# Kernel tuning notes

Measured on AMD Instinct MI355X. Metric: run time of the kernel, lower is better.

The kernel has to match this reference:

```python
import jax, jax.numpy as jnp
import numpy as np

B, N, D, H, NCTX = 4, 2048, 1024, 16, 512
HD = D // H  # head dim = 64


def setup_inputs() -> dict:
    key = jax.random.key(0)
    ks = jax.random.split(key, 6)
    return {
        "x": jax.random.normal(ks[0], (B, N, D), dtype=jnp.float32),
        "ctx_ppr": jax.random.uniform(ks[1], (B, NCTX), dtype=jnp.float32),
        "ctx_trust": jax.random.normal(ks[2], (B, NCTX), dtype=jnp.float32),
        "W_in": jax.random.normal(ks[3], (D, 3 * D), dtype=jnp.float32) * 0.02,
        "b_in": jnp.zeros((3 * D,), dtype=jnp.float32),
        "W_out": jax.random.normal(ks[4], (D, D), dtype=jnp.float32) * 0.02,
        "b_out": jnp.zeros((D,), dtype=jnp.float32),
        "log_ppr_alpha": jnp.full((1,), 0.1, dtype=jnp.float32),
        "trust_scale": jnp.full((1,), 0.1, dtype=jnp.float32),
        "n_ctx": NCTX,
    }


def reference(x, ctx_ppr, ctx_trust, W_in, b_in, W_out, b_out, log_ppr_alpha, trust_scale, n_ctx):
    b, n, dmodel = x.shape
    # QKV projection
    qkv = x @ W_in + b_in                                   # [B,N,3D]
    q, k, v = jnp.split(qkv, 3, axis=-1)
    q = q.reshape(b, n, H, HD).transpose(0, 2, 1, 3)        # [B,H,N,d]
    k = k.reshape(b, n, H, HD).transpose(0, 2, 1, 3)
    v = v.reshape(b, n, H, HD).transpose(0, 2, 1, 3)
    if n_ctx > 0:
        # multiplicative trust gate on context-token values
        gate = jax.nn.sigmoid(trust_scale * ctx_trust)      # [B,n_ctx]
        gate_full = jnp.concatenate(
            [gate, jnp.ones((b, n - n_ctx), dtype=x.dtype)], axis=1)  # [B,N]
        v = v * gate_full[:, None, :, None]
        # additive graph (log-PPR) column bias on attention logits
        col_bias = -log_ppr_alpha * jnp.log(jnp.maximum(ctx_ppr, 1e-8))  # [B,n_ctx]
        bias = jnp.concatenate(
            [col_bias, jnp.zeros((b, n - n_ctx), dtype=x.dtype)], axis=1)  # [B,N]
    else:
        bias = jnp.zeros((b, n), dtype=x.dtype)
    scale = 1.0 / np.sqrt(HD).astype(np.float32)
    scores = jnp.einsum("bhqd,bhkd->bhqk", q, k) * scale + bias[:, None, None, :]
    attn = jax.nn.softmax(scores, axis=-1)                  # [B,H,N,N]
    out = jnp.einsum("bhqk,bhkd->bhqd", attn, v)            # [B,H,N,d]
    out = out.transpose(0, 2, 1, 3).reshape(b, n, dmodel)
    return out @ W_out + b_out
```

## Files before the change

### kernel.cpp

```cpp
#include <hip/hip_runtime.h>
#include <hip/hip_bf16.h>
#include <stdint.h>

#define BATCH  4
#define NSEQ   2048
#define DMODEL 1024
#define NHEAD  16
#define HDIM   64
#define NCTXC  512

typedef unsigned short u16;
typedef __attribute__((ext_vector_type(8))) short bfrag;
typedef __attribute__((ext_vector_type(4))) float facc;

typedef __attribute__((address_space(3))) void lds_void;
typedef __attribute__((address_space(1))) void g_void;

__device__ __forceinline__ void gload16(const void* g, void* l) {
  __builtin_amdgcn_global_load_lds((const g_void*)g, (lds_void*)l, 16, 0, 0);
}

__device__ __forceinline__ u16 f2bf(float f) {
  uint32_t r;
  asm("v_cvt_pk_bf16_f32 %0, %1, %1" : "=v"(r) : "v"(f));
  return (u16)r;
}

#if __has_builtin(__builtin_amdgcn_cvt_pk_bf16_f32)
__device__ __forceinline__ uint32_t pk2bf(float a, float b) {
  return __builtin_bit_cast(uint32_t, __builtin_amdgcn_cvt_pk_bf16_f32(a, b));
}
#else
__device__ __forceinline__ uint32_t pk2bf(float a, float b) {
  uint32_t r;
  asm("v_cvt_pk_bf16_f32 %0, %1, %2" : "=v"(r) : "v"(a), "v"(b));
  return r;
}
#endif

__device__ __forceinline__ float bf2f(u16 h) {
  union { uint32_t u; float f; } un;
  un.u = ((uint32_t)h) << 16;
  return un.f;
}

__device__ __forceinline__ float load_flex(const void* p, size_t idx, int isb) {
  return isb ? bf2f(((const u16*)p)[idx]) : ((const float*)p)[idx];
}

__device__ __forceinline__ uint4 pack8(float4 a, float4 b) {
  uint4 r;
  r.x = pk2bf(a.x, a.y);
  r.y = pk2bf(a.z, a.w);
  r.z = pk2bf(b.x, b.y);
  r.w = pk2bf(b.z, b.w);
  return r;
}

__global__ __launch_bounds__(256) void detect_kernel(const u16* __restrict__ xraw,
                                                     int* __restrict__ flag) {
  __shared__ int s_high, s_zero;
  if (threadIdx.x == 0) { s_high = 0; s_zero = 0; }
  __syncthreads();
  int h = 0, z = 0;
  for (int i = threadIdx.x; i < 4096; i += 256) {
    const u16 v = xraw[2 * i];
    const int e = (v >> 7) & 0xFF;
    if (e >= 0x90) h++;
    if (v == 0) z++;
  }
  atomicAdd(&s_high, h);
  atomicAdd(&s_zero, z);
  __syncthreads();
  if (threadIdx.x == 0) flag[0] = (s_high < 64 && s_zero < 2048) ? 1 : 0;
}


__global__ __launch_bounds__(256) void cast_x_kernel(const void* __restrict__ x,
                                                     u16* __restrict__ xb,
                                                     const int* __restrict__ flag) {
  const int isb = flag[0];
  const int i = blockIdx.x * 256 + threadIdx.x;
  if (isb) {
    ((uint4*)xb)[i] = ((const uint4*)x)[i];
  } else {
    const float4 f0 = ((const float4*)x)[2 * i];
    const float4 f1 = ((const float4*)x)[2 * i + 1];
    ((uint4*)xb)[i] = pack8(f0, f1);
  }
}

__global__ __launch_bounds__(256) void transpose_flex(const void* __restrict__ W,
                                                      u16* __restrict__ Wt,
                                                      int R, int C,
                                                      const int* __restrict__ flag) {
  __shared__ float tile[32][33];
  const int isb = flag[0];
  const int tx = threadIdx.x;
  const int ty = threadIdx.y;
  const int c0 = blockIdx.x * 32;
  const int r0 = blockIdx.y * 32;
#pragma unroll
  for (int j = 0; j < 32; j += 8)
    tile[ty + j][tx] = load_flex(W, (size_t)(r0 + ty + j) * C + c0 + tx, isb);
  __syncthreads();
#pragma unroll
  for (int j = 0; j < 32; j += 8)
    Wt[(size_t)(c0 + ty + j) * R + r0 + tx] = f2bf(tile[tx][ty + j]);
}

__global__ __launch_bounds__(256) void prep_small(const void* __restrict__ b_in,
                                                  const void* __restrict__ b_out,
                                                  const void* __restrict__ ppr,
                                                  const void* __restrict__ trust,
                                                  const void* __restrict__ alpha_p,
                                                  const void* __restrict__ ts_p,
                                                  float* __restrict__ bin_f,
                                                  float* __restrict__ bout_f,
                                                  float* __restrict__ gate,
                                                  float* __restrict__ cbias,
                                                  const int* __restrict__ flag) {
  const int isb = flag[0];
  const int i = blockIdx.x * 256 + threadIdx.x;
  if (i < 3072) {
    bin_f[i] = load_flex(b_in, i, isb);
  } else if (i < 4096) {
    bout_f[i - 3072] = load_flex(b_out, i - 3072, isb);
  } else if (i < 4096 + BATCH * NCTXC) {
    const int j = i - 4096;
    const float ts = load_flex(ts_p, 0, isb), al = load_flex(alpha_p, 0, isb);
    gate[j]  = 1.0f / (1.0f + __expf(-ts * load_flex(trust, j, isb)));
    cbias[j] = -al * logf(fmaxf(load_flex(ppr, j, isb), 1e-8f)) * 1.44269504f;
  }
}

__device__ __forceinline__ void kloop_mfma(const u16* __restrict__ Ag,
                                           const u16* __restrict__ Bg,
                                           u16* As, u16* Bs,
                                           int tid, int wM, int wN, int l16, int quad,
                                           facc acc[4][4]) {
  char* ldsA = (char*)As + tid * 16;
  char* ldsB = (char*)Bs + tid * 16;
  for (int k0 = 0; k0 < 1024; k0 += 32) {
    __syncthreads();
    gload16(Ag + k0, ldsA);
    gload16(Ag + (size_t)64 * 1024 + k0, ldsA + 4096);
    gload16(Bg + k0, ldsB);
    gload16(Bg + (size_t)64 * 1024 + k0, ldsB + 4096);
    __syncthreads();

    bfrag af[4], bf[4];
#pragma unroll
    for (int i = 0; i < 4; ++i)
      af[i] = *(const bfrag*)(&As[(wM + i * 16 + l16) * 32 + quad * 8]);
#pragma unroll
    for (int j = 0; j < 4; ++j)
      bf[j] = *(const bfrag*)(&Bs[(wN + j * 16 + l16) * 32 + quad * 8]);
#pragma unroll
    for (int i = 0; i < 4; ++i)
#pragma unroll
      for (int j = 0; j < 4; ++j)
        acc[i][j] = __builtin_amdgcn_mfma_f32_16x16x32_bf16(af[i], bf[j], acc[i][j], 0, 0, 0);
  }
}

__global__ __launch_bounds__(256) void gemm_qkvt(const u16* __restrict__ xb,
                                                 const u16* __restrict__ Wt,
                                                 const float* __restrict__ bin_f,
                                                 const float* __restrict__ gate,
                                                 u16* __restrict__ qk,
                                                 u16* __restrict__ Vtg) {
  __shared__ u16 As[128 * 32];
  __shared__ u16 Bs[128 * 32];
  const int tid  = threadIdx.x;
  const int w    = tid >> 6;
  const int lane = tid & 63;
  const int quad = lane >> 4;
  const int l16  = lane & 15;
  const int wM   = (w >> 1) * 64;
  const int wN   = (w & 1) * 64;
  const int id   = blockIdx.x;
  const int srow  = tid >> 2;
  const int spart = tid & 3;

  facc acc[4][4] = {};

  if (id < 1024) {
    const int bn = id & 15, bm = id >> 4;
    const u16* Ag = xb + (size_t)(bm * 128 + srow) * 1024 + spart * 8;
    const u16* Bg = Wt + (size_t)(bn * 128 + srow) * 1024 + spart * 8;
    kloop_mfma(Ag, Bg, As, Bs, tid, wM, wN, l16, quad, acc);

    const float qs = (bn < 8) ? 0.18033688f : 1.0f;
#pragma unroll
    for (int i = 0; i < 4; ++i) {
      const int grow0 = bm * 128 + wM + i * 16 + quad * 4;
#pragma unroll
      for (int j = 0; j < 4; ++j) {
        const int gcol = bn * 128 + wN + j * 16 + l16;
        const float bv = bin_f[gcol];
#pragma unroll
        for (int r = 0; r < 4; ++r)
          qk[(size_t)(grow0 + r) * 2048 + gcol] = f2bf((acc[i][j][r] + bv) * qs);
      }
    }
  } else {
    const int id2 = id - 1024;
    const int bn = id2 & 63, bm = id2 >> 6;
    const u16* Ag = Wt + (size_t)2048 * 1024 + (size_t)(bm * 128 + srow) * 1024 + spart * 8;
    const u16* Bg = xb + (size_t)(bn * 128 + srow) * 1024 + spart * 8;
    kloop_mfma(Ag, Bg, As, Bs, tid, wM, wN, l16, quad, acc);

#pragma unroll
    for (int i = 0; i < 4; ++i) {
      const int grow0 = bm * 128 + wM + i * 16 + quad * 4;
      const int h   = grow0 >> 6;
      const int dd0 = grow0 & 63;
#pragma unroll
      for (int j = 0; j < 4; ++j) {
        const int gcol = bn * 128 + wN + j * 16 + l16;
        const int bb  = gcol >> 11;
        const int tok = gcol & (NSEQ - 1);
        const float gl = (tok < NCTXC) ? gate[bb * NCTXC + tok] : 1.0f;
        u16* dst = &Vtg[((size_t)((bb * NHEAD + h) * HDIM + dd0)) * NSEQ + tok];
#pragma unroll
        for (int r = 0; r < 4; ++r)
          dst[(size_t)r * NSEQ] = f2bf((acc[i][j][r] + bin_f[2 * DMODEL + grow0 + r]) * gl);
      }
    }
  }
}

__global__ __launch_bounds__(256) void gemm_out(const u16* __restrict__ A,
                                                const u16* __restrict__ Bt,
                                                const float* __restrict__ biasf,
                                                void* __restrict__ Cout,
                                                const int* __restrict__ flag) {
  __shared__ u16 As[128 * 32];
  __shared__ u16 Bs[128 * 32];
  const int isb  = flag[0];
  const int tid  = threadIdx.x;
  const int w    = tid >> 6;
  const int lane = tid & 63;
  const int quad = lane >> 4;
  const int l16  = lane & 15;
  const int wM   = (w >> 1) * 64;
  const int wN   = (w & 1) * 64;
  const int bm   = blockIdx.y;
  const int bn   = blockIdx.x;
  const int srow  = tid >> 2;
  const int spart = tid & 3;

  facc acc[4][4] = {};
  const u16* Ag = A + (size_t)(bm * 128 + srow) * 2048 + spart * 8;
  const u16* Bg = Bt + (size_t)(bn * 128 + srow) * 1024 + spart * 8;
  char* ldsA = (char*)As + tid * 16;
  char* ldsB = (char*)Bs + tid * 16;

  for (int k0 = 0; k0 < 1024; k0 += 32) {
    __syncthreads();
    gload16(Ag + k0, ldsA);
    gload16(Ag + (size_t)64 * 2048 + k0, ldsA + 4096);
    gload16(Bg + k0, ldsB);
    gload16(Bg + (size_t)64 * 1024 + k0, ldsB + 4096);
    __syncthreads();

    bfrag af[4], bf[4];
#pragma unroll
    for (int i = 0; i < 4; ++i)
      af[i] = *(const bfrag*)(&As[(wM + i * 16 + l16) * 32 + quad * 8]);
#pragma unroll
    for (int j = 0; j < 4; ++j)
      bf[j] = *(const bfrag*)(&Bs[(wN + j * 16 + l16) * 32 + quad * 8]);
#pragma unroll
    for (int i = 0; i < 4; ++i)
#pragma unroll
      for (int j = 0; j < 4; ++j)
        acc[i][j] = __builtin_amdgcn_mfma_f32_16x16x32_bf16(af[i], bf[j], acc[i][j], 0, 0, 0);
  }

#pragma unroll
  for (int i = 0; i < 4; ++i) {
    const int grow0 = bm * 128 + wM + i * 16 + quad * 4;
#pragma unroll
    for (int j = 0; j < 4; ++j) {
      const int gcol = bn * 128 + wN + j * 16 + l16;
      const float bv = biasf[gcol];
#pragma unroll
      for (int r = 0; r < 4; ++r) {
        const float v = acc[i][j][r] + bv;
        if (isb) ((u16*)Cout)[(size_t)(grow0 + r) * 1024 + gcol] = f2bf(v);
        else     ((float*)Cout)[(size_t)(grow0 + r) * 1024 + gcol] = v;
      }
    }
  }
}

__global__ __launch_bounds__(128, 2) void attn_kernel(u16* __restrict__ qk,
                                                      const u16* __restrict__ vtg,
                                                      const float* __restrict__ cbias) {
  const int id    = blockIdx.x;
  const int chunk = id >> 3;
  const int qt    = chunk & 15;
  const int hg    = (id & 7) | ((chunk >> 4) << 3);
  const int h     = hg & 15;
  const int b     = hg >> 4;

  __shared__ u16 KV[2][2][64 * 64];

  const int tid  = threadIdx.x;
  const int w    = tid >> 6;
  const int lane = tid & 63;
  const int quad = lane >> 4;
  const int l16  = lane & 15;

  bfrag bq[4][2];
#pragma unroll
  for (int qs = 0; qs < 4; ++qs) {
    const u16* qrow = qk + (size_t)(b * NSEQ + qt * 128 + w * 64 + qs * 16 + l16) * 2048 + h * HDIM;
    bq[qs][0] = *(const bfrag*)(qrow + quad * 8);
    bq[qs][1] = *(const bfrag*)(qrow + 32 + quad * 8);
  }

  bfrag ones;
#pragma unroll
  for (int i = 0; i < 8; ++i) ones[i] = (short)0x3F80;

  facc den[4] = {};
  facc o[4][4] = {};

  const u16* kbase = qk + (size_t)(b * NSEQ) * 2048 + DMODEL + h * HDIM;
  const u16* vbase = vtg + (size_t)((b * NHEAD + h) * HDIM) * NSEQ;

  int crow[4], csc[4];
#pragma unroll
  for (int i = 0; i < 4; ++i) {
    const int c = tid + i * 128;
    crow[i] = c >> 3;
    csc[i]  = (c & 7) ^ (crow[i] & 7);
  }

  const int e    = l16 & 7;
  const int swk0 = (quad ^ e) * 8;
  const int cA0  = ((quad >> 1) ^ e) * 8 + (quad & 1) * 4;

  auto stage = [&](int sel, int t) {
#pragma unroll
    for (int i = 0; i < 4; ++i) {
      const int c = tid + i * 128;
      gload16(kbase + (size_t)(t * 64 + crow[i]) * 2048 + csc[i] * 8, &KV[sel][0][c * 8]);
      gload16(vbase + (size_t)crow[i] * 2048 + t * 64 + csc[i] * 8,   &KV[sel][1][c * 8]);
    }
  };

  stage(0, 0);

  for (int t = 0; t < NSEQ / 64; ++t) {
    __syncthreads();
    if (t + 1 < NSEQ / 64) stage((t + 1) & 1, t + 1);

    const u16* Kb = KV[t & 1][0];
    const u16* Vb = KV[t & 1][1];

    bfrag ak[4][2];
#pragma unroll
    for (int nt = 0; nt < 4; ++nt) {
      const u16* kr = &Kb[(nt * 16 + l16) * 64];
      ak[nt][0] = *(const bfrag*)(kr + swk0);
      ak[nt][1] = *(const bfrag*)(kr + (swk0 ^ 32));
    }

    bfrag av[4][2];
#pragma unroll
    for (int dt = 0; dt < 4; ++dt) {
      const u16* vr = &Vb[(dt * 16 + l16) * 64];
      union { bfrag f; uint2 u2[2]; } un0, un1;
      un0.u2[0] = *(const uint2*)(vr + cA0);
      un0.u2[1] = *(const uint2*)(vr + (cA0 ^ 16));
      un1.u2[0] = *(const uint2*)(vr + (cA0 ^ 32));
      un1.u2[1] = *(const uint2*)(vr + (cA0 ^ 48));
      av[dt][0] = un0.f;
      av[dt][1] = un1.f;
    }

    facc zb[4];
    if (t < 8) {
      const float* cb = cbias + b * NCTXC + t * 64 + quad * 4;
#pragma unroll
      for (int nt = 0; nt < 4; ++nt) zb[nt] = *(const facc*)(cb + nt * 16);
    } else {
#pragma unroll
      for (int nt = 0; nt < 4; ++nt) zb[nt] = (facc){};
    }

#pragma unroll
    for (int qs = 0; qs < 4; ++qs) {
      facc s[4];
      __builtin_amdgcn_s_setprio(1);
#pragma unroll
      for (int nt = 0; nt < 4; ++nt) {
        facc z = zb[nt];
        z = __builtin_amdgcn_mfma_f32_16x16x32_bf16(ak[nt][0], bq[qs][0], z, 0, 0, 0);
        s[nt] = __builtin_amdgcn_mfma_f32_16x16x32_bf16(ak[nt][1], bq[qs][1], z, 0, 0, 0);
      }
      __builtin_amdgcn_s_setprio(0);

#pragma unroll
      for (int nt = 0; nt < 4; ++nt)
#pragma unroll
        for (int r = 0; r < 4; ++r)
          s[nt][r] = __builtin_amdgcn_exp2f(s[nt][r]);

      union { bfrag f; uint32_t wrd[4]; } bp0, bp1;
      bp0.wrd[0] = pk2bf(s[0][0], s[0][1]);
      bp0.wrd[1] = pk2bf(s[0][2], s[0][3]);
      bp0.wrd[2] = pk2bf(s[1][0], s[1][1]);
      bp0.wrd[3] = pk2bf(s[1][2], s[1][3]);
      bp1.wrd[0] = pk2bf(s[2][0], s[2][1]);
      bp1.wrd[1] = pk2bf(s[2][2], s[2][3]);
      bp1.wrd[2] = pk2bf(s[3][0], s[3][1]);
      bp1.wrd[3] = pk2bf(s[3][2], s[3][3]);

      __builtin_amdgcn_s_setprio(1);
#pragma unroll
      for (int dt = 0; dt < 4; ++dt) {
        o[qs][dt] = __builtin_amdgcn_mfma_f32_16x16x32_bf16(av[dt][0], bp0.f, o[qs][dt], 0, 0, 0);
        o[qs][dt] = __builtin_amdgcn_mfma_f32_16x16x32_bf16(av[dt][1], bp1.f, o[qs][dt], 0, 0, 0);
      }
      den[qs] = __builtin_amdgcn_mfma_f32_16x16x32_bf16(ones, bp0.f, den[qs], 0, 0, 0);
      den[qs] = __builtin_amdgcn_mfma_f32_16x16x32_bf16(ones, bp1.f, den[qs], 0, 0, 0);
      __builtin_amdgcn_s_setprio(0);
    }
  }

#pragma unroll
  for (int qs = 0; qs < 4; ++qs) {
    const float inv = 1.0f / den[qs][0];
    u16* orow = qk + (size_t)(b * NSEQ + qt * 128 + w * 64 + qs * 16 + l16) * 2048 + h * HDIM;
#pragma unroll
    for (int dt = 0; dt < 4; ++dt) {
      uint2 st;
      st.x = pk2bf(o[qs][dt][0] * inv, o[qs][dt][1] * inv);
      st.y = pk2bf(o[qs][dt][2] * inv, o[qs][dt][3] * inv);
      *(uint2*)(orow + dt * 16 + quad * 4) = st;
    }
  }
}


extern "C" void kernel_launch(void* const* d_in, const int* in_sizes, int n_in,
                              void* d_out, int out_size, void* d_ws, size_t ws_size,
                              hipStream_t stream) {
  const void* x          = d_in[0];
  const void* ctx_ppr    = d_in[1];
  const void* ctx_trust  = d_in[2];
  const void* W_in       = d_in[3];
  const void* b_in       = d_in[4];
  const void* W_out      = d_in[5];
  const void* b_out      = d_in[6];
  const void* lppr_alpha = d_in[7];
  const void* tscale     = d_in[8];

  char* ws = (char*)d_ws;
  u16* Wt    = (u16*)ws;  ws += (size_t)3072 * 1024 * 2;
  u16* WoT   = (u16*)ws;  ws += (size_t)1024 * 1024 * 2;
  u16* qk    = (u16*)ws;  ws += (size_t)8192 * 2048 * 2;
  u16* Vtg   = (u16*)ws;  ws += (size_t)64 * 64 * 2048 * 2;
  u16* xb    = (u16*)ws;  ws += (size_t)8192 * 1024 * 2;
  float* bin_f  = (float*)ws; ws += 3072 * 4;
  float* bout_f = (float*)ws; ws += 1024 * 4;
  float* gate   = (float*)ws; ws += (size_t)BATCH * NCTXC * 4;
  float* cbias  = (float*)ws; ws += (size_t)BATCH * NCTXC * 4;
  int*   flag   = (int*)ws;   ws += 64;

  detect_kernel<<<dim3(1), dim3(256), 0, stream>>>((const u16*)x, flag);
  cast_x_kernel<<<dim3(4096), dim3(256), 0, stream>>>(x, xb, flag);
  transpose_flex<<<dim3(96, 32), dim3(32, 8), 0, stream>>>(W_in, Wt, 1024, 3072, flag);
  transpose_flex<<<dim3(32, 32), dim3(32, 8), 0, stream>>>(W_out, WoT, 1024, 1024, flag);
  prep_small<<<dim3(24), dim3(256), 0, stream>>>(b_in, b_out, ctx_ppr, ctx_trust,
                                                 lppr_alpha, tscale,
                                                 bin_f, bout_f, gate, cbias, flag);
  gemm_qkvt<<<dim3(1536), dim3(256), 0, stream>>>(xb, Wt, bin_f, gate, qk, Vtg);
  attn_kernel<<<dim3(1024), dim3(128), 0, stream>>>(qk, Vtg, cbias);
  gemm_out<<<dim3(8, 64), dim3(256), 0, stream>>>(qk, WoT, bout_f, d_out, flag);
}
```

Baseline: 285.7 us.

## Switch projection GEMMs to 256x256 tiles with double-buffered swizzled LDS

Replaces the 128x128, 256-thread GEMM kernels for the QKV and output projections with 256x256 tiles on 512 threads (8 waves, 8x4 MFMA fragments each). Global-to-LDS loads are double-buffered so the next K slice is fetched while the current one is computed, which drops one barrier per iteration. LDS columns are XOR-swizzled to avoid bank conflicts, and MFMA sections are raised in priority. The larger tiles cut global/L2 traffic per flop but use more registers and give fewer blocks (384 and 128), which may leave the output GEMM underfilling the GPU's 256 CUs.

```diff
diff --git a/kernel.cpp b/kernel.cpp
--- a/kernel.cpp
+++ b/kernel.cpp
@@ -134,163 +134,145 @@
   }
 }
 
-__device__ __forceinline__ void kloop_mfma(const u16* __restrict__ Ag,
-                                           const u16* __restrict__ Bg,
-                                           u16* As, u16* Bs,
-                                           int tid, int wM, int wN, int l16, int quad,
-                                           facc acc[4][4]) {
-  char* ldsA = (char*)As + tid * 16;
-  char* ldsB = (char*)Bs + tid * 16;
-  for (int k0 = 0; k0 < 1024; k0 += 32) {
+__device__ __forceinline__ void gemm256_core(const u16* __restrict__ A, int lda,
+                                             const u16* __restrict__ B,
+                                             u16* __restrict__ LA, u16* __restrict__ LB,
+                                             int tid, facc acc[8][4]) {
+  const int lane = tid & 63, quad = lane >> 4, l16 = lane & 15;
+  const int w = tid >> 6, wm = w >> 2, wn = w & 3;
+  const int r = tid >> 2;
+  const int sA = (((tid & 3) ^ (r & 3) ^ ((r >> 2) & 3)) * 8);
+  const int xl = ((l16 & 3) ^ ((l16 >> 2) & 3));
+
+  const u16* a0 = A + (size_t)r * lda + sA;
+  const u16* b0 = B + (size_t)r * 1024 + sA;
+  char* dA = (char*)LA + tid * 16;
+  char* dB = (char*)LB + tid * 16;
+
+#pragma unroll
+  for (int h = 0; h < 2; ++h) {
+    gload16(a0 + (size_t)h * 128 * lda, dA + h * 8192);
+    gload16(b0 + (size_t)h * 128 * 1024, dB + h * 8192);
+  }
+
+  for (int kt = 0; kt < 32; ++kt) {
     __syncthreads();
-    gload16(Ag + k0, ldsA);
-    gload16(Ag + (size_t)64 * 1024 + k0, ldsA + 4096);
-    gload16(Bg + k0, ldsB);
-    gload16(Bg + (size_t)64 * 1024 + k0, ldsB + 4096);
-    __syncthreads();
-
-    bfrag af[4], bf[4];
-#pragma unroll
-    for (int i = 0; i < 4; ++i)
-      af[i] = *(const bfrag*)(&As[(wM + i * 16 + l16) * 32 + quad * 8]);
-#pragma unroll
-    for (int j = 0; j < 4; ++j)
-      bf[j] = *(const bfrag*)(&Bs[(wN + j * 16 + l16) * 32 + quad * 8]);
-#pragma unroll
-    for (int i = 0; i < 4; ++i)
-#pragma unroll
-      for (int j = 0; j < 4; ++j)
-        acc[i][j] = __builtin_amdgcn_mfma_f32_16x16x32_bf16(af[i], bf[j], acc[i][j], 0, 0, 0);
-  }
-}
-
-__global__ __launch_bounds__(256) void gemm_qkvt(const u16* __restrict__ xb,
-                                                 const u16* __restrict__ Wt,
-                                                 const float* __restrict__ bin_f,
-                                                 const float* __restrict__ gate,
-                                                 u16* __restrict__ qk,
-                                                 u16* __restrict__ Vtg) {
-  __shared__ u16 As[128 * 32];
-  __shared__ u16 Bs[128 * 32];
-  const int tid  = threadIdx.x;
-  const int w    = tid >> 6;
-  const int lane = tid & 63;
-  const int quad = lane >> 4;
-  const int l16  = lane & 15;
-  const int wM   = (w >> 1) * 64;
-  const int wN   = (w & 1) * 64;
-  const int id   = blockIdx.x;
-  const int srow  = tid >> 2;
-  const int spart = tid & 3;
-
-  facc acc[4][4] = {};
-
-  if (id < 1024) {
-    const int bn = id & 15, bm = id >> 4;
-    const u16* Ag = xb + (size_t)(bm * 128 + srow) * 1024 + spart * 8;
-    const u16* Bg = Wt + (size_t)(bn * 128 + srow) * 1024 + spart * 8;
-    kloop_mfma(Ag, Bg, As, Bs, tid, wM, wN, l16, quad, acc);
-
-    const float qs = (bn < 8) ? 0.18033688f : 1.0f;
-#pragma unroll
-    for (int i = 0; i < 4; ++i) {
-      const int grow0 = bm * 128 + wM + i * 16 + quad * 4;
-#pragma unroll
-      for (int j = 0; j < 4; ++j) {
-        const int gcol = bn * 128 + wN + j * 16 + l16;
+    const int par = kt & 1;
+    if (kt + 1 < 32) {
+      const int pn = par ^ 1;
+      const size_t ko = (size_t)(kt + 1) * 32;
+#pragma unroll
+      for (int h = 0; h < 2; ++h) {
+        gload16(a0 + (size_t)h * 128 * lda + ko, dA + pn * 16384 + h * 8192);
+        gload16(b0 + (size_t)h * 128 * 1024 + ko, dB + pn * 16384 + h * 8192);
+      }
+    }
+
+    const u16* Ab = LA + par * 8192;
+    const u16* Bb = LB + par * 8192;
+    bfrag af[8], bf[4];
+#pragma unroll
+    for (int mr = 0; mr < 8; ++mr)
+      af[mr] = *(const bfrag*)(&Ab[(wm * 128 + mr * 16 + l16) * 32 + ((quad ^ xl) * 8)]);
+#pragma unroll
+    for (int nr = 0; nr < 4; ++nr)
+      bf[nr] = *(const bfrag*)(&Bb[(wn * 64 + nr * 16 + l16) * 32 + ((quad ^ xl) * 8)]);
+
+    __builtin_amdgcn_s_setprio(1);
+#pragma unroll
+    for (int mr = 0; mr < 8; ++mr)
+#pragma unroll
+      for (int nr = 0; nr < 4; ++nr)
+        acc[mr][nr] = __builtin_amdgcn_mfma_f32_16x16x32_bf16(af[mr], bf[nr], acc[mr][nr], 0, 0, 0);
+    __builtin_amdgcn_s_setprio(0);
+  }
+}
+
+__global__ __launch_bounds__(512, 2) void gemm_qkvt256(const u16* __restrict__ xb,
+                                                       const u16* __restrict__ Wt,
+                                                       const float* __restrict__ bin_f,
+                                                       const float* __restrict__ gate,
+                                                       u16* __restrict__ qk,
+                                                       u16* __restrict__ Vtg) {
+  __shared__ u16 LA[2][8192];
+  __shared__ u16 LB[2][8192];
+  const int tid = threadIdx.x;
+  const int id  = blockIdx.x;
+  const int lane = tid & 63, quad = lane >> 4, l16 = lane & 15;
+  const int w = tid >> 6, wm = w >> 2, wn = w & 3;
+  facc acc[8][4] = {};
+
+  if (id < 256) {
+    const int bm = id >> 3, bn = id & 7;
+    gemm256_core(xb + (size_t)(bm * 256) * 1024, 1024,
+                 Wt + (size_t)(bn * 256) * 1024, &LA[0][0], &LB[0][0], tid, acc);
+    const float qs = (bn < 4) ? 0.18033688f : 1.0f;
+#pragma unroll
+    for (int mr = 0; mr < 8; ++mr) {
+      const int grow0 = bm * 256 + wm * 128 + mr * 16 + quad * 4;
+#pragma unroll
+      for (int nr = 0; nr < 4; ++nr) {
+        const int gcol = bn * 256 + wn * 64 + nr * 16 + l16;
         const float bv = bin_f[gcol];
 #pragma unroll
-        for (int r = 0; r < 4; ++r)
-          qk[(size_t)(grow0 + r) * 2048 + gcol] = f2bf((acc[i][j][r] + bv) * qs);
+        for (int rr = 0; rr < 4; ++rr)
+          qk[(size_t)(grow0 + rr) * 2048 + gcol] = f2bf((acc[mr][nr][rr] + bv) * qs);
       }
     }
   } else {
-    const int id2 = id - 1024;
-    const int bn = id2 & 63, bm = id2 >> 6;
-    const u16* Ag = Wt + (size_t)2048 * 1024 + (size_t)(bm * 128 + srow) * 1024 + spart * 8;
-    const u16* Bg = xb + (size_t)(bn * 128 + srow) * 1024 + spart * 8;
-    kloop_mfma(Ag, Bg, As, Bs, tid, wM, wN, l16, quad, acc);
-
-#pragma unroll
-    for (int i = 0; i < 4; ++i) {
-      const int grow0 = bm * 128 + wM + i * 16 + quad * 4;
-      const int h   = grow0 >> 6;
-      const int dd0 = grow0 & 63;
-#pragma unroll
-      for (int j = 0; j < 4; ++j) {
-        const int gcol = bn * 128 + wN + j * 16 + l16;
-        const int bb  = gcol >> 11;
-        const int tok = gcol & (NSEQ - 1);
+    const int id2 = id - 256;
+    const int bm = id2 >> 5, bn = id2 & 31;
+    gemm256_core(Wt + (size_t)2048 * 1024 + (size_t)(bm * 256) * 1024, 1024,
+                 xb + (size_t)(bn * 256) * 1024, &LA[0][0], &LB[0][0], tid, acc);
+#pragma unroll
+    for (int mr = 0; mr < 8; ++mr) {
+      const int grow0 = bm * 256 + wm * 128 + mr * 16 + quad * 4;
+#pragma unroll
+      for (int nr = 0; nr < 4; ++nr) {
+        const int gcol = bn * 256 + wn * 64 + nr * 16 + l16;
+        const int bb = gcol >> 11, tok = gcol & (NSEQ - 1);
         const float gl = (tok < NCTXC) ? gate[bb * NCTXC + tok] : 1.0f;
-        u16* dst = &Vtg[((size_t)((bb * NHEAD + h) * HDIM + dd0)) * NSEQ + tok];
-#pragma unroll
-        for (int r = 0; r < 4; ++r)
-          dst[(size_t)r * NSEQ] = f2bf((acc[i][j][r] + bin_f[2 * DMODEL + grow0 + r]) * gl);
-      }
-    }
-  }
-}
-
-__global__ __launch_bounds__(256) void gemm_out(const u16* __restrict__ A,
-                                                const u16* __restrict__ Bt,
-                                                const float* __restrict__ biasf,
-                                                void* __restrict__ Cout,
-                                                const int* __restrict__ flag) {
-  __shared__ u16 As[128 * 32];
-  __shared__ u16 Bs[128 * 32];
-  const int isb  = flag[0];
-  const int tid  = threadIdx.x;
-  const int w    = tid >> 6;
-  const int lane = tid & 63;
-  const int quad = lane >> 4;
-  const int l16  = lane & 15;
-  const int wM   = (w >> 1) * 64;
-  const int wN   = (w & 1) * 64;
-  const int bm   = blockIdx.y;
-  const int bn   = blockIdx.x;
-  const int srow  = tid >> 2;
-  const int spart = tid & 3;
-
-  facc acc[4][4] = {};
-  const u16* Ag = A + (size_t)(bm * 128 + srow) * 2048 + spart * 8;
-  const u16* Bg = Bt + (size_t)(bn * 128 + srow) * 1024 + spart * 8;
-  char* ldsA = (char*)As + tid * 16;
-  char* ldsB = (char*)Bs + tid * 16;
-
-  for (int k0 = 0; k0 < 1024; k0 += 32) {
-    __syncthreads();
-    gload16(Ag + k0, ldsA);
-    gload16(Ag + (size_t)64 * 2048 + k0, ldsA + 4096);
-    gload16(Bg + k0, ldsB);
-    gload16(Bg + (size_t)64 * 1024 + k0, ldsB + 4096);
-    __syncthreads();
-
-    bfrag af[4], bf[4];
-#pragma unroll
-    for (int i = 0; i < 4; ++i)
-      af[i] = *(const bfrag*)(&As[(wM + i * 16 + l16) * 32 + quad * 8]);
-#pragma unroll
-    for (int j = 0; j < 4; ++j)
-      bf[j] = *(const bfrag*)(&Bs[(wN + j * 16 + l16) * 32 + quad * 8]);
-#pragma unroll
-    for (int i = 0; i < 4; ++i)
-#pragma unroll
-      for (int j = 0; j < 4; ++j)
-        acc[i][j] = __builtin_amdgcn_mfma_f32_16x16x32_bf16(af[i], bf[j], acc[i][j], 0, 0, 0);
-  }
-
-#pragma unroll
-  for (int i = 0; i < 4; ++i) {
-    const int grow0 = bm * 128 + wM + i * 16 + quad * 4;
-#pragma unroll
-    for (int j = 0; j < 4; ++j) {
-      const int gcol = bn * 128 + wN + j * 16 + l16;
+#pragma unroll
+        for (int rr = 0; rr < 4; ++rr) {
+          const int grow = grow0 + rr;
+          const int h = grow >> 6, dd = grow & 63;
+          Vtg[((size_t)((bb * NHEAD + h) * HDIM + dd)) * NSEQ + tok] =
+              f2bf((acc[mr][nr][rr] + bin_f[2 * DMODEL + grow]) * gl);
+        }
+      }
+    }
+  }
+}
+
+__global__ __launch_bounds__(512, 2) void gemm_out256(const u16* __restrict__ A,
+                                                      const u16* __restrict__ Bt,
+                                                      const float* __restrict__ biasf,
+                                                      void* __restrict__ Cout,
+                                                      const int* __restrict__ flag) {
+  __shared__ u16 LA[2][8192];
+  __shared__ u16 LB[2][8192];
+  const int tid = threadIdx.x;
+  const int isb = flag[0];
+  const int bm = blockIdx.x >> 2, bn = blockIdx.x & 3;
+  const int lane = tid & 63, quad = lane >> 4, l16 = lane & 15;
+  const int w = tid >> 6, wm = w >> 2, wn = w & 3;
+  facc acc[8][4] = {};
+
+  gemm256_core(A + (size_t)(bm * 256) * 2048, 2048,
+               Bt + (size_t)(bn * 256) * 1024, &LA[0][0], &LB[0][0], tid, acc);
+
+#pragma unroll
+  for (int mr = 0; mr < 8; ++mr) {
+    const int grow0 = bm * 256 + wm * 128 + mr * 16 + quad * 4;
+#pragma unroll
+    for (int nr = 0; nr < 4; ++nr) {
+      const int gcol = bn * 256 + wn * 64 + nr * 16 + l16;
       const float bv = biasf[gcol];
 #pragma unroll
-      for (int r = 0; r < 4; ++r) {
-        const float v = acc[i][j][r] + bv;
-        if (isb) ((u16*)Cout)[(size_t)(grow0 + r) * 1024 + gcol] = f2bf(v);
-        else     ((float*)Cout)[(size_t)(grow0 + r) * 1024 + gcol] = v;
+      for (int rr = 0; rr < 4; ++rr) {
+        const float v = acc[mr][nr][rr] + bv;
+        if (isb) ((u16*)Cout)[(size_t)(grow0 + rr) * 1024 + gcol] = f2bf(v);
+        else     ((float*)Cout)[(size_t)(grow0 + rr) * 1024 + gcol] = v;
       }
     }
   }
@@ -480,7 +462,7 @@
   prep_small<<<dim3(24), dim3(256), 0, stream>>>(b_in, b_out, ctx_ppr, ctx_trust,
                                                  lppr_alpha, tscale,
                                                  bin_f, bout_f, gate, cbias, flag);
-  gemm_qkvt<<<dim3(1536), dim3(256), 0, stream>>>(xb, Wt, bin_f, gate, qk, Vtg);
+  gemm_qkvt256<<<dim3(384), dim3(512), 0, stream>>>(xb, Wt, bin_f, gate, qk, Vtg);
   attn_kernel<<<dim3(1024), dim3(128), 0, stream>>>(qk, Vtg, cbias);
-  gemm_out<<<dim3(8, 64), dim3(256), 0, stream>>>(qk, WoT, bout_f, d_out, flag);
-}
+  gemm_out256<<<dim3(128), dim3(512), 0, stream>>>(qk, WoT, bout_f, d_out, flag);
+}
```

Measured after the change: 332.4 us. 16.3% more time.
